# Optimization experiments

Hardware: AMD Instinct MI355X
Metric: run time of the kernel (lower is better)

The kernel has to match this reference:

```python
import jax, jax.numpy as jnp
import numpy as np

N_NODES = 10000
N_EDGES = 80000
IN_DIM = 1024
HID = 4096
OUT = 256


def sage_conv(x, src, dst, W_l, b_l, W_r, num_nodes):
    # mean aggregation of source-node features onto target nodes
    msg = x[src]                                            # [E, D] gather
    agg = jax.ops.segment_sum(msg, dst, num_segments=num_nodes)   # [N, D]
    cnt = jax.ops.segment_sum(jnp.ones((src.shape[0],), x.dtype), dst,
                              num_segments=num_nodes)       # [N]
    mean = agg / jnp.clip(cnt, 1.0)[:, None]                # isolated nodes -> 0
    # lin_l(mean) + lin_r(x); lin_r has no bias in PyG SAGEConv
    return mean @ W_l.T + b_l + x @ W_r.T


def setup_inputs() -> dict:
    key = jax.random.key(0)
    ks = jax.random.split(key, 6)
    x = jax.random.normal(ks[0], (N_NODES, IN_DIM), dtype=jnp.float32)
    edge_index = jax.random.randint(ks[1], (2, N_EDGES), 0, N_NODES, dtype=jnp.int32)
    s1 = 1.0 / np.sqrt(IN_DIM)
    s2 = 1.0 / np.sqrt(HID)
    W1_l = jax.random.normal(ks[2], (HID, IN_DIM), dtype=jnp.float32) * s1
    b1_l = jnp.zeros((HID,), jnp.float32)
    W1_r = jax.random.normal(ks[3], (HID, IN_DIM), dtype=jnp.float32) * s1
    W2_l = jax.random.normal(ks[4], (OUT, HID), dtype=jnp.float32) * s2
    b2_l = jnp.zeros((OUT,), jnp.float32)
    W2_r = jax.random.normal(ks[5], (OUT, HID), dtype=jnp.float32) * s2
    return {"x": x, "edge_index": edge_index, "W1_l": W1_l, "b1_l": b1_l,
            "W1_r": W1_r, "W2_l": W2_l, "b2_l": b2_l, "W2_r": W2_r}


def reference(x, edge_index, W1_l, b1_l, W1_r, W2_l, b2_l, W2_r):
    src, dst = edge_index[0], edge_index[1]
    h = sage_conv(x, src, dst, W1_l, b1_l, W1_r, N_NODES)   # [N, 4096]
    h = jax.nn.relu(h)
    # dropout is identity in eval mode
    out = sage_conv(h, src, dst, W2_l, b2_l, W2_r, N_NODES)  # [N, 256]
    return jax.nn.log_softmax(out, axis=1)
```

## Files before the change

### kernel.cpp

```cpp
#include <hip/hip_runtime.h>
#include <cstdint>
#include <cstddef>

#define DEVINL __device__ __forceinline__

typedef __bf16 bf16x8 __attribute__((ext_vector_type(8)));
typedef float f32x4 __attribute__((ext_vector_type(4)));

static constexpr int NN = 10000;
static constexpr int NE = 80000;
static constexpr int IN_DIM = 1024;
static constexpr int HID = 4096;
static constexpr int OUTD = 256;
static constexpr int M_PAD = 10112;

DEVINL unsigned short f2bf(float f) {
  unsigned int u = __builtin_bit_cast(unsigned int, f);
  u += 0x7fffu + ((u >> 16) & 1u);
  return (unsigned short)(u >> 16);
}
DEVINL float bf2f(unsigned short h) {
  unsigned int u = ((unsigned int)h) << 16;
  return __builtin_bit_cast(float, u);
}

DEVINL void ld_lds16(const void* g, void* l) {
  __builtin_amdgcn_global_load_lds(
      (const __attribute__((address_space(1))) unsigned int*)g,
      (__attribute__((address_space(3))) unsigned int*)l, 16, 0, 0);
}

static constexpr int PREP_B1 = 8192;
static constexpr int PREP_B2 = PREP_B1 + 2048;
static constexpr int PREP_B3 = PREP_B2 + 10000;
static constexpr int PREP_NB = PREP_B3 + 313;

__global__ __launch_bounds__(256) void prep_kernel(
    const float* __restrict__ W1l, const float* __restrict__ W1r,
    const float* __restrict__ W2l, const float* __restrict__ W2r,
    const float* __restrict__ x, const int* __restrict__ dst,
    unsigned short* __restrict__ w1cat, unsigned short* __restrict__ w2cat,
    unsigned short* __restrict__ x_bf, int* __restrict__ deg) {
  int b = blockIdx.x;
  int t = threadIdx.x;
  if (b < PREP_B1) {
    int g = b * 256 + t;
    int n = g >> 9;
    int kg = g & 511;
    const float* s = (kg < 256) ? (W1l + (size_t)n * 1024 + kg * 4)
                                : (W1r + (size_t)n * 1024 + (kg - 256) * 4);
    float4 v = *(const float4*)s;
    ushort4 p = {f2bf(v.x), f2bf(v.y), f2bf(v.z), f2bf(v.w)};
    ((ushort4*)w1cat)[g] = p;
  } else if (b < PREP_B2) {
    int g = (b - PREP_B1) * 256 + t;
    int n = g >> 10;
    int kg = g & 1023;
    const float* s = (n < 256) ? (W2l + (size_t)n * 4096 + kg * 4)
                               : (W2r + (size_t)(n - 256) * 4096 + kg * 4);
    float4 v = *(const float4*)s;
    ushort4 p = {f2bf(v.x), f2bf(v.y), f2bf(v.z), f2bf(v.w)};
    ((ushort4*)w2cat)[g] = p;
  } else if (b < PREP_B3) {
    int g = (b - PREP_B2) * 256 + t;
    int i = g >> 8;
    int kg = g & 255;
    float4 v = ((const float4*)(x + (size_t)i * IN_DIM))[kg];
    ushort4 p = {f2bf(v.x), f2bf(v.y), f2bf(v.z), f2bf(v.w)};
    ((ushort4*)(x_bf + (size_t)i * IN_DIM))[kg] = p;
  } else {
    int e = (b - PREP_B3) * 256 + t;
    if (e < NE) atomicAdd(&deg[dst[e]], 1);
  }
}

__global__ __launch_bounds__(256) void scan_kernel(const int* __restrict__ deg,
                                                   int* __restrict__ offs,
                                                   int* __restrict__ cur) {
  __shared__ int part[256];
  constexpr int NPT = 40;
  int t = threadIdx.x;
  int base = t * NPT;
  int s = 0;
  for (int j = 0; j < NPT; ++j) {
    int n = base + j;
    s += (n < NN) ? deg[n] : 0;
  }
  part[t] = s;
  __syncthreads();
  for (int o = 1; o < 256; o <<= 1) {
    int v = (t >= o) ? part[t - o] : 0;
    __syncthreads();
    part[t] += v;
    __syncthreads();
  }
  int pre = (t > 0) ? part[t - 1] : 0;
  for (int j = 0; j < NPT; ++j) {
    int n = base + j;
    if (n < NN) {
      offs[n] = pre;
      cur[n] = pre;
      pre += deg[n];
    }
  }
  if (t == 255) offs[NN] = part[255];
}

__global__ void bin_kernel(const int* __restrict__ src, const int* __restrict__ dst,
                           int* __restrict__ cur, int* __restrict__ csr) {
  int e = blockIdx.x * 256 + threadIdx.x;
  if (e < NE) {
    int p = atomicAdd(&cur[dst[e]], 1);
    csr[p] = src[e];
  }
}

__global__ __launch_bounds__(256) void gather1_kernel(const unsigned short* __restrict__ x_bf,
                                                      const int* __restrict__ offs,
                                                      const int* __restrict__ csr,
                                                      unsigned short* __restrict__ A1) {
  int i = blockIdx.x;
  int t = threadIdx.x;
  unsigned short* row = A1 + (size_t)i * 2048;
  if (i >= NN) {
    ushort4 z = {0, 0, 0, 0};
    ((ushort4*)row)[t] = z;
    ((ushort4*)(row + 1024))[t] = z;
    return;
  }
  int beg = offs[i], end = offs[i + 1];
  float4 a0 = {0.f, 0.f, 0.f, 0.f}, a1 = {0.f, 0.f, 0.f, 0.f};
  int j = beg;
  for (; j + 2 <= end; j += 2) {
    int s0 = __builtin_amdgcn_readfirstlane(csr[j]);
    int s1 = __builtin_amdgcn_readfirstlane(csr[j + 1]);
    ushort4 u0 = ((const ushort4*)(x_bf + (size_t)s0 * IN_DIM))[t];
    ushort4 u1 = ((const ushort4*)(x_bf + (size_t)s1 * IN_DIM))[t];
    a0.x += bf2f(u0.x); a0.y += bf2f(u0.y); a0.z += bf2f(u0.z); a0.w += bf2f(u0.w);
    a1.x += bf2f(u1.x); a1.y += bf2f(u1.y); a1.z += bf2f(u1.z); a1.w += bf2f(u1.w);
  }
  if (j < end) {
    int s0 = __builtin_amdgcn_readfirstlane(csr[j]);
    ushort4 u0 = ((const ushort4*)(x_bf + (size_t)s0 * IN_DIM))[t];
    a0.x += bf2f(u0.x); a0.y += bf2f(u0.y); a0.z += bf2f(u0.z); a0.w += bf2f(u0.w);
  }
  float inv = 1.0f / (float)max(end - beg, 1);
  ushort4 ub = ((const ushort4*)(x_bf + (size_t)i * IN_DIM))[t];
  ushort4 pa = {f2bf((a0.x + a1.x) * inv), f2bf((a0.y + a1.y) * inv),
                f2bf((a0.z + a1.z) * inv), f2bf((a0.w + a1.w) * inv)};
  ((ushort4*)row)[t] = pa;
  ((ushort4*)(row + 1024))[t] = ub;
}

template <int BM, int BK, int K, int N, int NUMM, int NUMN, int GM, int EPI>
__global__ __launch_bounds__(256) void gemm_kernel(const unsigned short* __restrict__ A,
                                                   const unsigned short* __restrict__ Bt,
                                                   const float* __restrict__ bias,
                                                   void* __restrict__ C0out,
                                                   void* __restrict__ C1out) {
  constexpr int BN = 128;
  constexpr int MI = BM / 32;
  constexpr int NI = 4;
  constexpr int CPR = BK / 8;
  constexpr int SA = BM * CPR / 256;
  constexpr int SB = BN * CPR / 256;
  constexpr int KK = BK / 32;
  __shared__ unsigned short Asm[BM * BK];
  __shared__ unsigned short Bsm[BN * BK];

  constexpr int NPG = GM * NUMN;
  const int pid = blockIdx.x;
  const int gid = pid / NPG;
  const int first_m = gid * GM;
  const int sz = (NUMM - first_m < GM) ? (NUMM - first_m) : GM;
  const int local = pid % NPG;
  const int pm = first_m + local % sz;
  const int pn = local / sz;

  const int tid = threadIdx.x;
  const int lane = tid & 63;
  const int wave = tid >> 6;
  const int quad = lane >> 4;
  const int l16 = lane & 15;
  const int wm = (wave & 1) * (BM / 2);
  const int wn = (wave >> 1) * 64;
  const long tm0 = (long)pm * BM;
  const long tn0 = (long)pn * BN;

  f32x4 acc[MI][NI];
#pragma unroll
  for (int i = 0; i < MI; ++i)
#pragma unroll
    for (int j = 0; j < NI; ++j) acc[i][j] = (f32x4){0.f, 0.f, 0.f, 0.f};

  const unsigned short* aSrc[SA];
  unsigned short* aDst[SA];
  const unsigned short* bSrc[SB];
  unsigned short* bDst[SB];
#pragma unroll
  for (int s = 0; s < SA; ++s) {
    int c = s * 256 + wave * 64 + lane;
    int r = c / CPR;
    int g = (c % CPR) ^ (r & 7);
    aSrc[s] = A + (size_t)(tm0 + r) * K + g * 8;
    aDst[s] = Asm + s * 2048 + wave * 512;
  }
#pragma unroll
  for (int s = 0; s < SB; ++s) {
    int c = s * 256 + wave * 64 + lane;
    int r = c / CPR;
    int g = (c % CPR) ^ (r & 7);
    bSrc[s] = Bt + (size_t)(tn0 + r) * K + g * 8;
    bDst[s] = Bsm + s * 2048 + wave * 512;
  }

  const int l7 = l16 & 7;

  for (int k0 = 0; k0 < K; k0 += BK) {
#pragma unroll
    for (int s = 0; s < SA; ++s) ld_lds16(aSrc[s] + k0, aDst[s]);
#pragma unroll
    for (int s = 0; s < SB; ++s) ld_lds16(bSrc[s] + k0, bDst[s]);
    __syncthreads();

#pragma unroll
    for (int kk = 0; kk < KK; ++kk) {
      const int p = (kk * 4 + quad) ^ l7;
      bf16x8 af[MI], bv[NI];
#pragma unroll
      for (int i = 0; i < MI; ++i) {
        int ra = wm + i * 16 + l16;
        af[i] = *(const bf16x8*)(Asm + ra * BK + p * 8);
      }
#pragma unroll
      for (int j = 0; j < NI; ++j) {
        int rb = wn + j * 16 + l16;
        bv[j] = *(const bf16x8*)(Bsm + rb * BK + p * 8);
      }
#pragma unroll
      for (int i = 0; i < MI; ++i)
#pragma unroll
        for (int j = 0; j < NI; ++j)
          acc[i][j] = __builtin_amdgcn_mfma_f32_16x16x32_bf16(af[i], bv[j], acc[i][j], 0, 0, 0);
    }
    __syncthreads();
  }

  if (EPI == 1) {
    unsigned short* C = (unsigned short*)C0out;
#pragma unroll
    for (int i = 0; i < MI; ++i) {
      long m0 = tm0 + wm + i * 16 + quad * 4;
#pragma unroll
      for (int j = 0; j < NI; ++j) {
        int n = (int)tn0 + wn + j * 16 + l16;
        float bvs = bias[n];
#pragma unroll
        for (int r = 0; r < 4; ++r) {
          float v = acc[i][j][r] + bvs;
          v = fmaxf(v, 0.0f);
          C[(size_t)(m0 + r) * N + n] = f2bf(v);
        }
      }
    }
  } else {
    unsigned short* PL = (unsigned short*)C0out;
    float* PR = (float*)C1out;
#pragma unroll
    for (int i = 0; i < MI; ++i) {
      long m0 = tm0 + wm + i * 16 + quad * 4;
#pragma unroll
      for (int j = 0; j < NI; ++j) {
        int n = (int)tn0 + wn + j * 16 + l16;
        if (n < 256) {
#pragma unroll
          for (int r = 0; r < 4; ++r) PL[(size_t)(m0 + r) * 256 + n] = f2bf(acc[i][j][r]);
        } else {
#pragma unroll
          for (int r = 0; r < 4; ++r) PR[(size_t)(m0 + r) * 256 + (n - 256)] = acc[i][j][r];
        }
      }
    }
  }
}

__global__ __launch_bounds__(128) void gather2_final_kernel(const unsigned short* __restrict__ pl,
                                                            const float* __restrict__ pr,
                                                            const int* __restrict__ offs,
                                                            const int* __restrict__ csr,
                                                            const float* __restrict__ b2,
                                                            float* __restrict__ out) {
  int i = blockIdx.x;
  int t = threadIdx.x;
  int beg = offs[i], end = offs[i + 1];
  float a0 = 0.f, a1 = 0.f, c0 = 0.f, c1 = 0.f;
  int j = beg;
  for (; j + 2 <= end; j += 2) {
    int s0 = __builtin_amdgcn_readfirstlane(csr[j]);
    int s1 = __builtin_amdgcn_readfirstlane(csr[j + 1]);
    unsigned int u0 = ((const unsigned int*)(pl + (size_t)s0 * 256))[t];
    unsigned int u1 = ((const unsigned int*)(pl + (size_t)s1 * 256))[t];
    a0 += bf2f((unsigned short)(u0 & 0xffffu));
    a1 += bf2f((unsigned short)(u0 >> 16));
    c0 += bf2f((unsigned short)(u1 & 0xffffu));
    c1 += bf2f((unsigned short)(u1 >> 16));
  }
  if (j < end) {
    int s0 = __builtin_amdgcn_readfirstlane(csr[j]);
    unsigned int u0 = ((const unsigned int*)(pl + (size_t)s0 * 256))[t];
    a0 += bf2f((unsigned short)(u0 & 0xffffu));
    a1 += bf2f((unsigned short)(u0 >> 16));
  }
  float inv = 1.0f / (float)max(end - beg, 1);
  float2 bv = ((const float2*)b2)[t];
  float2 pv = ((const float2*)(pr + (size_t)i * 256))[t];
  float v0 = (a0 + c0) * inv + bv.x + pv.x;
  float v1 = (a1 + c1) * inv + bv.y + pv.y;

  __shared__ float sm[2], ss[2];
  int w = t >> 6;
  float m = fmaxf(v0, v1);
#pragma unroll
  for (int o = 32; o > 0; o >>= 1) m = fmaxf(m, __shfl_xor(m, o, 64));
  if ((t & 63) == 0) sm[w] = m;
  __syncthreads();
  m = fmaxf(sm[0], sm[1]);

  float s = __expf(v0 - m) + __expf(v1 - m);
#pragma unroll
  for (int o = 32; o > 0; o >>= 1) s += __shfl_xor(s, o, 64);
  if ((t & 63) == 0) ss[w] = s;
  __syncthreads();
  float ls = logf(ss[0] + ss[1]);

  float2 o2 = {v0 - m - ls, v1 - m - ls};
  ((float2*)(out + (size_t)i * OUTD))[t] = o2;
}

static constexpr size_t OFF_A1 = 0;
static constexpr size_t OFF_W1 = OFF_A1 + (size_t)M_PAD * 2048 * 2;
static constexpr size_t OFF_HB = OFF_W1 + (size_t)HID * 2048 * 2;
static constexpr size_t OFF_W2 = OFF_HB + (size_t)M_PAD * HID * 2;
static constexpr size_t OFF_XBF = OFF_W2 - (size_t)NN * IN_DIM * 2;
static constexpr size_t OFF_DEG = OFF_W2 + (size_t)512 * HID * 2;
static constexpr size_t OFF_OFFS = OFF_DEG + (size_t)NN * 4;
static constexpr size_t OFF_CUR = OFF_OFFS + (size_t)(NN + 4) * 4;
static constexpr size_t OFF_CSR = OFF_CUR + (size_t)NN * 4;
static constexpr size_t OFF_PL = OFF_A1;
static constexpr size_t OFF_PR = OFF_PL + (size_t)M_PAD * 256 * 2;

extern "C" void kernel_launch(void* const* d_in, const int* in_sizes, int n_in,
                              void* d_out, int out_size, void* d_ws, size_t ws_size,
                              hipStream_t stream) {
  const float* x = (const float*)d_in[0];
  const int* ei = (const int*)d_in[1];
  const int* src = ei;
  const int* dst = ei + NE;
  const float* W1_l = (const float*)d_in[2];
  const float* b1_l = (const float*)d_in[3];
  const float* W1_r = (const float*)d_in[4];
  const float* W2_l = (const float*)d_in[5];
  const float* b2_l = (const float*)d_in[6];
  const float* W2_r = (const float*)d_in[7];
  float* out = (float*)d_out;

  char* ws = (char*)d_ws;
  unsigned short* A1 = (unsigned short*)(ws + OFF_A1);
  unsigned short* w1cat = (unsigned short*)(ws + OFF_W1);
  unsigned short* h_b = (unsigned short*)(ws + OFF_HB);
  unsigned short* x_bf = (unsigned short*)(ws + OFF_XBF);
  unsigned short* w2cat = (unsigned short*)(ws + OFF_W2);
  int* deg = (int*)(ws + OFF_DEG);
  int* offs = (int*)(ws + OFF_OFFS);
  int* cur = (int*)(ws + OFF_CUR);
  int* csr = (int*)(ws + OFF_CSR);
  unsigned short* pl = (unsigned short*)(ws + OFF_PL);
  float* pr = (float*)(ws + OFF_PR);

  hipMemsetAsync(deg, 0, (size_t)NN * 4, stream);

  prep_kernel<<<PREP_NB, 256, 0, stream>>>(W1_l, W1_r, W2_l, W2_r, x, dst,
                                           w1cat, w2cat, x_bf, deg);
  scan_kernel<<<1, 256, 0, stream>>>(deg, offs, cur);
  bin_kernel<<<(NE + 255) / 256, 256, 0, stream>>>(src, dst, cur, csr);

  gather1_kernel<<<M_PAD, 256, 0, stream>>>(x_bf, offs, csr, A1);

  gemm_kernel<128, 64, 2048, 4096, 79, 32, 32, 1>
      <<<79 * 32, 256, 0, stream>>>(A1, w1cat, b1_l, h_b, nullptr);
  gemm_kernel<64, 128, 4096, 512, 158, 4, 64, 2>
      <<<158 * 4, 256, 0, stream>>>(h_b, w2cat, nullptr, pl, pr);

  gather2_final_kernel<<<NN, 128, 0, stream>>>(pl, pr, offs, csr, b2_l, out);
}
```

Measured before the change: 444.0 us.

## Split-K the second GEMM into two halves and reduce with a new kernel

```diff
diff --git a/kernel.cpp b/kernel.cpp
--- a/kernel.cpp
+++ b/kernel.cpp
@@ -152,12 +152,11 @@
   ((ushort4*)(row + 1024))[t] = ub;
 }
 
-template <int BM, int BK, int K, int N, int NUMM, int NUMN, int GM, int EPI>
+template <int BM, int BK, int K, int KSPLIT, int N, int NUMM, int NUMN, int GM, int EPI>
 __global__ __launch_bounds__(256) void gemm_kernel(const unsigned short* __restrict__ A,
                                                    const unsigned short* __restrict__ Bt,
                                                    const float* __restrict__ bias,
-                                                   void* __restrict__ C0out,
-                                                   void* __restrict__ C1out) {
+                                                   void* __restrict__ C0out) {
   constexpr int BN = 128;
   constexpr int MI = BM / 32;
   constexpr int NI = 4;
@@ -165,6 +164,7 @@
   constexpr int SA = BM * CPR / 256;
   constexpr int SB = BN * CPR / 256;
   constexpr int KK = BK / 32;
+  constexpr int KS = K / KSPLIT;
   __shared__ unsigned short Asm[BM * BK];
   __shared__ unsigned short Bsm[BN * BK];
 
@@ -176,6 +176,7 @@
   const int local = pid % NPG;
   const int pm = first_m + local % sz;
   const int pn = local / sz;
+  const int koff = (KSPLIT > 1) ? (int)blockIdx.y * KS : 0;
 
   const int tid = threadIdx.x;
   const int lane = tid & 63;
@@ -202,7 +203,7 @@
     int c = s * 256 + wave * 64 + lane;
     int r = c / CPR;
     int g = (c % CPR) ^ (r & 7);
-    aSrc[s] = A + (size_t)(tm0 + r) * K + g * 8;
+    aSrc[s] = A + (size_t)(tm0 + r) * K + koff + g * 8;
     aDst[s] = Asm + s * 2048 + wave * 512;
   }
 #pragma unroll
@@ -210,13 +211,13 @@
     int c = s * 256 + wave * 64 + lane;
     int r = c / CPR;
     int g = (c % CPR) ^ (r & 7);
-    bSrc[s] = Bt + (size_t)(tn0 + r) * K + g * 8;
+    bSrc[s] = Bt + (size_t)(tn0 + r) * K + koff + g * 8;
     bDst[s] = Bsm + s * 2048 + wave * 512;
   }
 
   const int l7 = l16 & 7;
 
-  for (int k0 = 0; k0 < K; k0 += BK) {
+  for (int k0 = 0; k0 < KS; k0 += BK) {
 #pragma unroll
     for (int s = 0; s < SA; ++s) ld_lds16(aSrc[s] + k0, aDst[s]);
 #pragma unroll
@@ -264,23 +265,47 @@
       }
     }
   } else {
-    unsigned short* PL = (unsigned short*)C0out;
-    float* PR = (float*)C1out;
+    unsigned short* C = (unsigned short*)C0out + (size_t)blockIdx.y * NUMM * BM * N;
 #pragma unroll
     for (int i = 0; i < MI; ++i) {
       long m0 = tm0 + wm + i * 16 + quad * 4;
 #pragma unroll
       for (int j = 0; j < NI; ++j) {
         int n = (int)tn0 + wn + j * 16 + l16;
-        if (n < 256) {
-#pragma unroll
-          for (int r = 0; r < 4; ++r) PL[(size_t)(m0 + r) * 256 + n] = f2bf(acc[i][j][r]);
-        } else {
-#pragma unroll
-          for (int r = 0; r < 4; ++r) PR[(size_t)(m0 + r) * 256 + (n - 256)] = acc[i][j][r];
-        }
+#pragma unroll
+        for (int r = 0; r < 4; ++r) C[(size_t)(m0 + r) * N + n] = f2bf(acc[i][j][r]);
       }
     }
+  }
+}
+
+__global__ __launch_bounds__(256) void reduce2_kernel(const unsigned short* __restrict__ P,
+                                                      unsigned short* __restrict__ pl,
+                                                      float* __restrict__ pr) {
+  int tid = threadIdx.x;
+  size_t row = (size_t)blockIdx.x * 4 + (tid >> 6);
+  int col = (tid & 63) * 8;
+  size_t base = row * 512 + col;
+  uint4 a = *(const uint4*)(P + base);
+  uint4 b = *(const uint4*)(P + (size_t)M_PAD * 512 + base);
+  float s[8];
+  const unsigned int* aw = (const unsigned int*)&a;
+  const unsigned int* bw = (const unsigned int*)&b;
+#pragma unroll
+  for (int j = 0; j < 4; ++j) {
+    s[2 * j] = bf2f((unsigned short)(aw[j] & 0xffffu)) + bf2f((unsigned short)(bw[j] & 0xffffu));
+    s[2 * j + 1] = bf2f((unsigned short)(aw[j] >> 16)) + bf2f((unsigned short)(bw[j] >> 16));
+  }
+  if (col < 256) {
+    unsigned int o[4];
+#pragma unroll
+    for (int j = 0; j < 4; ++j)
+      o[j] = (unsigned int)f2bf(s[2 * j]) | ((unsigned int)f2bf(s[2 * j + 1]) << 16);
+    *(uint4*)(pl + row * 256 + col) = *(const uint4*)o;
+  } else {
+    float* d = pr + row * 256 + (col - 256);
+    *(float4*)d = (float4){s[0], s[1], s[2], s[3]};
+    *(float4*)(d + 4) = (float4){s[4], s[5], s[6], s[7]};
   }
 }
 
@@ -346,7 +371,8 @@
 static constexpr size_t OFF_OFFS = OFF_DEG + (size_t)NN * 4;
 static constexpr size_t OFF_CUR = OFF_OFFS + (size_t)(NN + 4) * 4;
 static constexpr size_t OFF_CSR = OFF_CUR + (size_t)NN * 4;
-static constexpr size_t OFF_PL = OFF_A1;
+static constexpr size_t OFF_P = OFF_A1;
+static constexpr size_t OFF_PL = OFF_P + (size_t)2 * M_PAD * 512 * 2;
 static constexpr size_t OFF_PR = OFF_PL + (size_t)M_PAD * 256 * 2;
 
 extern "C" void kernel_launch(void* const* d_in, const int* in_sizes, int n_in,
@@ -374,6 +400,7 @@
   int* offs = (int*)(ws + OFF_OFFS);
   int* cur = (int*)(ws + OFF_CUR);
   int* csr = (int*)(ws + OFF_CSR);
+  unsigned short* P = (unsigned short*)(ws + OFF_P);
   unsigned short* pl = (unsigned short*)(ws + OFF_PL);
   float* pr = (float*)(ws + OFF_PR);
 
@@ -386,10 +413,11 @@
 
   gather1_kernel<<<M_PAD, 256, 0, stream>>>(x_bf, offs, csr, A1);
 
-  gemm_kernel<128, 64, 2048, 4096, 79, 32, 32, 1>
-      <<<79 * 32, 256, 0, stream>>>(A1, w1cat, b1_l, h_b, nullptr);
-  gemm_kernel<64, 128, 4096, 512, 158, 4, 64, 2>
-      <<<158 * 4, 256, 0, stream>>>(h_b, w2cat, nullptr, pl, pr);
+  gemm_kernel<128, 64, 2048, 1, 4096, 79, 32, 32, 1>
+      <<<79 * 32, 256, 0, stream>>>(A1, w1cat, b1_l, h_b);
+  gemm_kernel<64, 128, 4096, 2, 512, 158, 4, 64, 3>
+      <<<dim3(158 * 4, 2), 256, 0, stream>>>(h_b, w2cat, nullptr, P);
+  reduce2_kernel<<<M_PAD / 4, 256, 0, stream>>>(P, pl, pr);
 
   gather2_final_kernel<<<NN, 128, 0, stream>>>(pl, pr, offs, csr, b2_l, out);
 }
```

After: 444.3 us. No clear change (+0.1%).
